# Performance work log

Measured on AMD Instinct MI355X. Metric: run time of the kernel, lower is better.

## Reference

```python
import jax, jax.numpy as jnp
import numpy as np

NUM_HEADS = 8


def setup_inputs() -> dict:
    key = jax.random.key(0)
    ks = jax.random.split(key, 14)
    B, S, E = 4, 2048, 512
    D_EMO = 64
    s = 1.0 / np.sqrt(E)
    inp = {
        "query": jax.random.normal(ks[0], (B, S, E), jnp.float32),
        "key": jax.random.normal(ks[1], (B, S, E), jnp.float32),
        "value": jax.random.normal(ks[2], (B, S, E), jnp.float32),
        "emotional_context": jax.random.normal(ks[3], (B, D_EMO), jnp.float32),
        "Wq": jax.random.normal(ks[4], (E, E), jnp.float32) * s,
        "bq": jnp.zeros((E,), jnp.float32),
        "Wk": jax.random.normal(ks[5], (E, E), jnp.float32) * s,
        "bk": jnp.zeros((E,), jnp.float32),
        "Wv": jax.random.normal(ks[6], (E, E), jnp.float32) * s,
        "bv": jnp.zeros((E,), jnp.float32),
        "Wo": jax.random.normal(ks[7], (E, E), jnp.float32) * s,
        "bo": jnp.zeros((E,), jnp.float32),
        "emo_bias": jax.random.normal(ks[8], (NUM_HEADS, 1, 1), jnp.float32),
    }
    return inp


def reference(query, key, value, emotional_context, Wq, bq, Wk, bk, Wv, bv, Wo, bo, emo_bias):
    B, S, E = query.shape
    H = NUM_HEADS
    D = E // H
    scale = 1.0 / np.sqrt(D).astype(np.float32)

    def proj(x, W, b):  # [B,S,E] -> [B,H,S,D]
        return (x @ W.T + b).reshape(B, S, H, D).transpose(0, 2, 1, 3)

    Q = proj(query, Wq, bq)
    K = proj(key, Wk, bk)
    V = proj(value, Wv, bv)

    # [B,H,S,S] score tensor (the memory-bound hot spot)
    scores = jnp.einsum("bhqd,bhkd->bhqk", Q, K) * scale
    scores = scores + emo_bias[None]  # additive per-head emotional bias
    # multiplicative emotional modulation: sigmoid of mean context, per batch
    mod = 0.5 + 0.5 * jax.nn.sigmoid(emotional_context.mean(axis=-1))  # [B]
    scores = scores * mod[:, None, None, None]

    attn = jax.nn.softmax(scores, axis=-1)
    # dropout(0.1) is identity in eval mode
    attended = jnp.einsum("bhqk,bhkd->bhqd", attn, V)
    attended = attended.transpose(0, 2, 1, 3).reshape(B, S, E)
    output = attended @ Wo.T + bo
    return output, attn.mean(axis=1)
```

## Files before the change

kernel.cpp:

```cpp
#include <hip/hip_runtime.h>

#define BATCH 4
#define SEQ   2048
#define EMB   512
#define HEADS 8
#define HD    64

typedef _Float16 half2_t __attribute__((ext_vector_type(2)));
typedef _Float16 half4_t __attribute__((ext_vector_type(4)));
typedef _Float16 half8_t __attribute__((ext_vector_type(8)));
typedef float    f32x4   __attribute__((ext_vector_type(4)));

#if __has_builtin(__builtin_amdgcn_exp2f)
#define EXP2F(x) __builtin_amdgcn_exp2f(x)
#else
#define EXP2F(x) exp2f(x)
#endif
#define LOG2E 1.44269504088896f

#define PKRTZ(a, b) __builtin_bit_cast(half2_t, __builtin_amdgcn_cvt_pkrtz((a), (b)))

__global__ void mod_kernel(const float* __restrict__ emo, float* __restrict__ modv){
    int lane = threadIdx.x;
    for (int b = 0; b < BATCH; ++b){
        float v = emo[b*64 + lane];
        #pragma unroll
        for (int off = 32; off >= 1; off >>= 1) v += __shfl_xor(v, off, 64);
        if (lane == 0){
            float mean = v * (1.0f/64.0f);
            float sig  = 1.0f/(1.0f + __expf(-mean));
            modv[b] = 0.5f + 0.5f*sig;
        }
    }
}

__device__ inline half8_t cvt8(const float* p){
    float4 v0 = *(const float4*)p;
    float4 v1 = *(const float4*)(p + 4);
    half8_t r;
    r[0]=(_Float16)v0.x; r[1]=(_Float16)v0.y; r[2]=(_Float16)v0.z; r[3]=(_Float16)v0.w;
    r[4]=(_Float16)v1.x; r[5]=(_Float16)v1.y; r[6]=(_Float16)v1.z; r[7]=(_Float16)v1.w;
    return r;
}

__global__ __launch_bounds__(256) void qkv_kernel(
    const float* __restrict__ X0, const float* __restrict__ X1, const float* __restrict__ X2,
    const float* __restrict__ W0, const float* __restrict__ W1, const float* __restrict__ W2,
    const float* __restrict__ b0, const float* __restrict__ b1, const float* __restrict__ b2,
    _Float16* __restrict__ o0, _Float16* __restrict__ o1, _Float16* __restrict__ o2)
{
    const int z = blockIdx.z;
    const float* X    = (z==0) ? X0 : (z==1) ? X1 : X2;
    const float* W    = (z==0) ? W0 : (z==1) ? W1 : W2;
    const float* bias = (z==0) ? b0 : (z==1) ? b1 : b2;
    _Float16*  out    = (z==0) ? o0 : (z==1) ? o1 : o2;

    __shared__ _Float16 lA[128*64];
    __shared__ _Float16 lB[64*64];

    const int tid  = threadIdx.x;
    const int wid  = tid >> 6;
    const int lane = tid & 63;
    const int l16  = lane & 15;
    const int g    = lane >> 4;
    const int l7   = l16 & 7;
    const int mb = blockIdx.x;
    const int nb = blockIdx.y;
    const int wm = (wid >> 1)*64;
    const int wn = (wid & 1)*32;
    const int tR = tid >> 3;
    const int c8 = tid & 7;

    f32x4 acc[4][2] = {};
    for (int ks = 0; ks < 8; ++ks){
        __syncthreads();
        #pragma unroll
        for (int p = 0; p < 4; ++p){
            const int R = p*32 + tR;
            half8_t h = cvt8(X + (size_t)(mb*128 + R)*EMB + ks*64 + c8*8);
            *(half8_t*)(lA + R*64 + ((c8 ^ (R & 7))*8)) = h;
        }
        #pragma unroll
        for (int p = 0; p < 2; ++p){
            const int R = p*32 + tR;
            half8_t h = cvt8(W + (size_t)(nb*64 + R)*EMB + ks*64 + c8*8);
            *(half8_t*)(lB + R*64 + ((c8 ^ (R & 7))*8)) = h;
        }
        __syncthreads();
        #pragma unroll
        for (int u = 0; u < 2; ++u){
            half8_t af[4], bf[2];
            #pragma unroll
            for (int i = 0; i < 4; ++i){
                const int rA = wm + i*16 + l16;
                af[i] = *(half8_t*)(lA + rA*64 + (((u*4 + g) ^ l7)*8));
            }
            #pragma unroll
            for (int j = 0; j < 2; ++j){
                const int rB = wn + j*16 + l16;
                bf[j] = *(half8_t*)(lB + rB*64 + (((u*4 + g) ^ l7)*8));
            }
            #pragma unroll
            for (int i = 0; i < 4; ++i)
                #pragma unroll
                for (int j = 0; j < 2; ++j)
                    acc[i][j] = __builtin_amdgcn_mfma_f32_16x16x32_f16(af[i], bf[j], acc[i][j], 0, 0, 0);
        }
    }
    #pragma unroll
    for (int j = 0; j < 2; ++j){
        const int nn  = nb*64 + wn + j*16 + l16;
        const float bn = bias[nn];
        const int h = nn >> 6, d = nn & 63;
        #pragma unroll
        for (int i = 0; i < 4; ++i){
            #pragma unroll
            for (int r = 0; r < 4; ++r){
                const int m  = mb*128 + wm + i*16 + 4*g + r;
                const int bb2 = m >> 11, s = m & 2047;
                const int bh  = bb2*8 + h;
                const float v = acc[i][j][r] + bn;
                size_t idx;
                if (z == 2)
                    idx = ((size_t)(bh*128 + (s>>4))*2 + (d>>5))*512
                        + (size_t)((((s>>2)&3)*16 + (d&15))*8 + ((d>>4)&1)*4 + (s&3));
                else
                    idx = ((size_t)(bh*128 + (s>>4))*2 + (d>>5))*512
                        + (size_t)((((d>>3)&3)*16 + (s&15))*8 + (d&7));
                out[idx] = (_Float16)v;
            }
        }
    }
}

__global__ __launch_bounds__(256) void pv_kernel(
    const _Float16* __restrict__ Qf, const _Float16* __restrict__ Kf,
    const _Float16* __restrict__ Vf, const float* __restrict__ emo_bias,
    const float* __restrict__ modv, _Float16* __restrict__ attended,
    float* __restrict__ Ldenom)
{
    __shared__ _Float16 lK[2][4096];
    __shared__ _Float16 lV[2][4096];

    const int tid  = threadIdx.x;
    const int lane = tid & 63;
    const int l16  = lane & 15;
    const int g    = lane >> 4;
    const int w    = tid >> 6;
    const int n    = blockIdx.x;
    const int work = (n & 7)*128 + (n >> 3);
    const int qt   = work & 31;
    const int bh   = work >> 5;
    const int b    = bh >> 3, h = bh & 7;
    const int q0   = qt*64 + w*16;

    const float mod = modv[b];
    const float sm2 = 0.125f * mod * LOG2E;
    const float bm2 = emo_bias[h] * mod * LOG2E;

    const size_t fB = (size_t)bh * 128;

    half8_t qf[2];
    #pragma unroll
    for (int c = 0; c < 2; ++c)
        qf[c] = *(const half8_t*)(Qf + ((fB + (q0>>4))*2 + c)*512 + lane*8);

    {
        const _Float16* gk = Kf + (fB)*1024 + tid*16;
        const _Float16* gv = Vf + (fB)*1024 + tid*16;
        *(half8_t*)(&lK[0][tid*16])     = *(const half8_t*)(gk);
        *(half8_t*)(&lK[0][tid*16 + 8]) = *(const half8_t*)(gk + 8);
        *(half8_t*)(&lV[0][tid*16])     = *(const half8_t*)(gv);
        *(half8_t*)(&lV[0][tid*16 + 8]) = *(const half8_t*)(gv + 8);
    }
    __syncthreads();

    f32x4 acc[4] = {};
    float lsum = 0.f;
    int cur = 0;
    for (int grp = 0; grp < SEQ/64; ++grp){
        half8_t rk0, rk1, rv0, rv1;
        if (grp < SEQ/64 - 1){
            const _Float16* gk = Kf + (fB + (size_t)(grp+1)*4)*1024 + tid*16;
            const _Float16* gv = Vf + (fB + (size_t)(grp+1)*4)*1024 + tid*16;
            rk0 = *(const half8_t*)(gk);
            rk1 = *(const half8_t*)(gk + 8);
            rv0 = *(const half8_t*)(gv);
            rv1 = *(const half8_t*)(gv + 8);
        }
        const _Float16* kb = &lK[cur][0];
        const _Float16* vb = &lV[cur][0];
        #pragma unroll
        for (int t = 0; t < 4; ++t){
            half8_t k0 = *(const half8_t*)(kb + (t*2+0)*512 + lane*8);
            half8_t k1 = *(const half8_t*)(kb + (t*2+1)*512 + lane*8);
            f32x4 s = {};
            s = __builtin_amdgcn_mfma_f32_16x16x32_f16(k0, qf[0], s, 0, 0, 0);
            s = __builtin_amdgcn_mfma_f32_16x16x32_f16(k1, qf[1], s, 0, 0, 0);
            float e0 = EXP2F(s[0]*sm2 + bm2);
            float e1 = EXP2F(s[1]*sm2 + bm2);
            float e2 = EXP2F(s[2]*sm2 + bm2);
            float e3 = EXP2F(s[3]*sm2 + bm2);
            lsum += (e0 + e1) + (e2 + e3);
            half2_t plo = PKRTZ(e0, e1), phi = PKRTZ(e2, e3);
            half4_t pf  = __builtin_shufflevector(plo, phi, 0, 1, 2, 3);
            half8_t vp0 = *(const half8_t*)(vb + (t*2+0)*512 + lane*8);
            half8_t vp1 = *(const half8_t*)(vb + (t*2+1)*512 + lane*8);
            half4_t v0 = __builtin_shufflevector(vp0, vp0, 0, 1, 2, 3);
            half4_t v1 = __builtin_shufflevector(vp0, vp0, 4, 5, 6, 7);
            half4_t v2 = __builtin_shufflevector(vp1, vp1, 0, 1, 2, 3);
            half4_t v3 = __builtin_shufflevector(vp1, vp1, 4, 5, 6, 7);
            acc[0] = __builtin_amdgcn_mfma_f32_16x16x16f16(pf, v0, acc[0], 0, 0, 0);
            acc[1] = __builtin_amdgcn_mfma_f32_16x16x16f16(pf, v1, acc[1], 0, 0, 0);
            acc[2] = __builtin_amdgcn_mfma_f32_16x16x16f16(pf, v2, acc[2], 0, 0, 0);
            acc[3] = __builtin_amdgcn_mfma_f32_16x16x16f16(pf, v3, acc[3], 0, 0, 0);
        }
        if (grp < SEQ/64 - 1){
            _Float16* dk = &lK[cur^1][tid*16];
            _Float16* dv = &lV[cur^1][tid*16];
            *(half8_t*)(dk)     = rk0;
            *(half8_t*)(dk + 8) = rk1;
            *(half8_t*)(dv)     = rv0;
            *(half8_t*)(dv + 8) = rv1;
        }
        __syncthreads();
        cur ^= 1;
    }

    lsum += __shfl_xor(lsum, 16, 64);
    lsum += __shfl_xor(lsum, 32, 64);
    if (g == 0) Ldenom[(size_t)bh*SEQ + q0 + l16] = lsum;
    const float inv = 1.0f / lsum;
    float invr[4];
    #pragma unroll
    for (int r = 0; r < 4; ++r)
        invr[r] = __shfl(inv, 4*g + r, 64);
    #pragma unroll
    for (int c = 0; c < 4; ++c)
        #pragma unroll
        for (int r = 0; r < 4; ++r)
            attended[(size_t)(b*SEQ + q0 + 4*g + r)*EMB + h*64 + 16*c + l16]
                = (_Float16)(acc[c][r] * invr[r]);
}

__global__ __launch_bounds__(256) void mean_kernel(
    const _Float16* __restrict__ Qf, const _Float16* __restrict__ Kf,
    const float* __restrict__ emo_bias, const float* __restrict__ modv,
    const float* __restrict__ Ldenom, float* __restrict__ mean_out)
{
    const int tid  = threadIdx.x;
    const int w    = tid >> 6;
    const int lane = tid & 63;
    const int l16  = lane & 15;
    const int g    = lane >> 4;
    const int n    = blockIdx.x;
    const int work = (n & 7)*512 + (n >> 3);
    const int b    = work >> 10;
    const int ky   = (work >> 7) & 7;
    const int qt   = work & 127;
    const int q0   = qt * 16;
    const int k0w  = ky*256 + w*64;

    const float mod = modv[b];
    const float sm2 = 0.125f * mod * LOG2E;

    f32x4 msum[4] = {};
    for (int hp = 0; hp < HEADS/2; ++hp){
        const int h0 = 2*hp, h1 = 2*hp + 1;
        const size_t lo0 = (size_t)(b*HEADS + h0) * SEQ;
        const size_t lo1 = (size_t)(b*HEADS + h1) * SEQ;
        const size_t f0  = (size_t)(b*HEADS + h0) * 128;
        const size_t f1  = (size_t)(b*HEADS + h1) * 128;
        const float bm20 = emo_bias[h0] * mod * LOG2E;
        const float bm21 = emo_bias[h1] * mod * LOG2E;
        half8_t qa0 = *(const half8_t*)(Qf + ((f0 + (q0>>4))*2 + 0)*512 + lane*8);
        half8_t qa1 = *(const half8_t*)(Qf + ((f0 + (q0>>4))*2 + 1)*512 + lane*8);
        half8_t qb0 = *(const half8_t*)(Qf + ((f1 + (q0>>4))*2 + 0)*512 + lane*8);
        half8_t qb1 = *(const half8_t*)(Qf + ((f1 + (q0>>4))*2 + 1)*512 + lane*8);
        float iA[4], iB[4];
        #pragma unroll
        for (int r = 0; r < 4; ++r){
            iA[r] = 1.0f / Ldenom[lo0 + q0 + 4*g + r];
            iB[r] = 1.0f / Ldenom[lo1 + q0 + 4*g + r];
        }
        #pragma unroll
        for (int j = 0; j < 4; ++j){
            const int kc = (k0w >> 4) + j;
            half8_t ka0 = *(const half8_t*)(Kf + ((f0 + kc)*2 + 0)*512 + lane*8);
            half8_t ka1 = *(const half8_t*)(Kf + ((f0 + kc)*2 + 1)*512 + lane*8);
            half8_t kb0 = *(const half8_t*)(Kf + ((f1 + kc)*2 + 0)*512 + lane*8);
            half8_t kb1 = *(const half8_t*)(Kf + ((f1 + kc)*2 + 1)*512 + lane*8);
            f32x4 sA = {}, sB = {};
            sA = __builtin_amdgcn_mfma_f32_16x16x32_f16(qa0, ka0, sA, 0, 0, 0);
            sA = __builtin_amdgcn_mfma_f32_16x16x32_f16(qa1, ka1, sA, 0, 0, 0);
            sB = __builtin_amdgcn_mfma_f32_16x16x32_f16(qb0, kb0, sB, 0, 0, 0);
            sB = __builtin_amdgcn_mfma_f32_16x16x32_f16(qb1, kb1, sB, 0, 0, 0);
            #pragma unroll
            for (int r = 0; r < 4; ++r){
                float pa = EXP2F(sA[r]*sm2 + bm20) * iA[r];
                float pb = EXP2F(sB[r]*sm2 + bm21) * iB[r];
                msum[j][r] += pa + pb;
            }
        }
    }
    #pragma unroll
    for (int j = 0; j < 4; ++j)
        #pragma unroll
        for (int r = 0; r < 4; ++r)
            mean_out[(size_t)(b*SEQ + q0 + 4*g + r)*SEQ + k0w + j*16 + l16]
                = msum[j][r] * (1.0f/HEADS);
}

__global__ __launch_bounds__(256) void outproj_kernel(
    const _Float16* __restrict__ A, const float* __restrict__ W,
    const float* __restrict__ bias, float* __restrict__ out)
{
    __shared__ _Float16 lA[128*64];
    __shared__ _Float16 lB[64*64];

    const int tid  = threadIdx.x;
    const int wid  = tid >> 6;
    const int lane = tid & 63;
    const int l16  = lane & 15;
    const int g    = lane >> 4;
    const int l7   = l16 & 7;
    const int mb = blockIdx.x;
    const int nb = blockIdx.y;
    const int wm = (wid >> 1)*64;
    const int wn = (wid & 1)*32;
    const int tR = tid >> 3;
    const int c8 = tid & 7;

    f32x4 acc[4][2] = {};
    for (int ks = 0; ks < 8; ++ks){
        __syncthreads();
        #pragma unroll
        for (int p = 0; p < 4; ++p){
            const int R = p*32 + tR;
            half8_t h = *(const half8_t*)(A + (size_t)(mb*128 + R)*EMB + ks*64 + c8*8);
            *(half8_t*)(lA + R*64 + ((c8 ^ (R & 7))*8)) = h;
        }
        #pragma unroll
        for (int p = 0; p < 2; ++p){
            const int R = p*32 + tR;
            half8_t h = cvt8(W + (size_t)(nb*64 + R)*EMB + ks*64 + c8*8);
            *(half8_t*)(lB + R*64 + ((c8 ^ (R & 7))*8)) = h;
        }
        __syncthreads();
        #pragma unroll
        for (int u = 0; u < 2; ++u){
            half8_t af[4], bf[2];
            #pragma unroll
            for (int i = 0; i < 4; ++i){
                const int rA = wm + i*16 + l16;
                af[i] = *(half8_t*)(lA + rA*64 + (((u*4 + g) ^ l7)*8));
            }
            #pragma unroll
            for (int j = 0; j < 2; ++j){
                const int rB = wn + j*16 + l16;
                bf[j] = *(half8_t*)(lB + rB*64 + (((u*4 + g) ^ l7)*8));
            }
            #pragma unroll
            for (int i = 0; i < 4; ++i)
                #pragma unroll
                for (int j = 0; j < 2; ++j)
                    acc[i][j] = __builtin_amdgcn_mfma_f32_16x16x32_f16(af[i], bf[j], acc[i][j], 0, 0, 0);
        }
    }
    #pragma unroll
    for (int j = 0; j < 2; ++j){
        const int nn = nb*64 + wn + j*16 + l16;
        const float bn = bias[nn];
        #pragma unroll
        for (int i = 0; i < 4; ++i)
            #pragma unroll
            for (int r = 0; r < 4; ++r){
                const int m = mb*128 + wm + i*16 + 4*g + r;
                out[(size_t)m*EMB + nn] = acc[i][j][r] + bn;
            }
    }
}

extern "C" void kernel_launch(void* const* d_in, const int* in_sizes, int n_in,
                              void* d_out, int out_size, void* d_ws, size_t ws_size,
                              hipStream_t stream)
{
    const float* query = (const float*)d_in[0];
    const float* key_  = (const float*)d_in[1];
    const float* value = (const float*)d_in[2];
    const float* emo   = (const float*)d_in[3];
    const float* Wq = (const float*)d_in[4];
    const float* bq = (const float*)d_in[5];
    const float* Wk = (const float*)d_in[6];
    const float* bk = (const float*)d_in[7];
    const float* Wv = (const float*)d_in[8];
    const float* bv = (const float*)d_in[9];
    const float* Wo = (const float*)d_in[10];
    const float* bo = (const float*)d_in[11];
    const float* emo_bias = (const float*)d_in[12];

    const size_t NTOK = (size_t)BATCH * SEQ * EMB;
    _Float16* ws       = (_Float16*)d_ws;
    _Float16* Qp       = ws;
    _Float16* Kp       = ws + NTOK;
    _Float16* Vt       = ws + 2*NTOK;
    _Float16* attended = ws + 3*NTOK;

    float* out0     = (float*)d_out;
    float* mean_out = out0 + NTOK;
    float* Ldenom   = out0;
    float* modv     = out0 + (size_t)BATCH*HEADS*SEQ;

    mod_kernel<<<1, 64, 0, stream>>>(emo, modv);
    qkv_kernel<<<dim3(64, 8, 3), 256, 0, stream>>>(query, key_, value, Wq, Wk, Wv,
                                                   bq, bk, bv, Qp, Kp, Vt);
    pv_kernel<<<BATCH*HEADS*(SEQ/64), 256, 0, stream>>>(Qp, Kp, Vt, emo_bias, modv, attended, Ldenom);
    mean_kernel<<<BATCH*(SEQ/16)*(SEQ/256), 256, 0, stream>>>(Qp, Kp, emo_bias, modv, Ldenom, mean_out);
    outproj_kernel<<<dim3(64, 8), 256, 0, stream>>>(attended, Wo, bo, out0);
}
```

Baseline: 177.2 us.

## Double-buffer LDS tiles in projection GEMMs and coalesce K/V tile loads

The QKV and output-projection GEMMs now use two LDS buffers and prefetch the next K-slice from global memory into registers while MFMAs run on the current slice. This removes one barrier per iteration and hides global load latency behind compute. In the attention kernel, the K/V tile copy is reorganised so consecutive threads read consecutive 16-byte chunks (tid*8 and tid*8+2048) instead of 32-byte strided pairs, which should improve coalescing. The GEMMs double their LDS use and raise register pressure, which may lower occupancy.

Measured after the change: 177.3 us. No clear change (+0.1%).

```diff
diff --git a/kernel.cpp b/kernel.cpp
--- a/kernel.cpp
+++ b/kernel.cpp
@@ -37,6 +37,13 @@
 __device__ inline half8_t cvt8(const float* p){
     float4 v0 = *(const float4*)p;
     float4 v1 = *(const float4*)(p + 4);
+    half8_t r;
+    r[0]=(_Float16)v0.x; r[1]=(_Float16)v0.y; r[2]=(_Float16)v0.z; r[3]=(_Float16)v0.w;
+    r[4]=(_Float16)v1.x; r[5]=(_Float16)v1.y; r[6]=(_Float16)v1.z; r[7]=(_Float16)v1.w;
+    return r;
+}
+
+__device__ inline half8_t cvt8v(float4 v0, float4 v1){
     half8_t r;
     r[0]=(_Float16)v0.x; r[1]=(_Float16)v0.y; r[2]=(_Float16)v0.z; r[3]=(_Float16)v0.w;
     r[4]=(_Float16)v1.x; r[5]=(_Float16)v1.y; r[6]=(_Float16)v1.z; r[7]=(_Float16)v1.w;
@@ -55,8 +62,8 @@
     const float* bias = (z==0) ? b0 : (z==1) ? b1 : b2;
     _Float16*  out    = (z==0) ? o0 : (z==1) ? o1 : o2;
 
-    __shared__ _Float16 lA[128*64];
-    __shared__ _Float16 lB[64*64];
+    __shared__ _Float16 lA[2][128*64];
+    __shared__ _Float16 lB[2][64*64];
 
     const int tid  = threadIdx.x;
     const int wid  = tid >> 6;
@@ -71,34 +78,50 @@
     const int tR = tid >> 3;
     const int c8 = tid & 7;
 
+    #pragma unroll
+    for (int p = 0; p < 4; ++p){
+        const int R = p*32 + tR;
+        half8_t h = cvt8(X + (size_t)(mb*128 + R)*EMB + c8*8);
+        *(half8_t*)(&lA[0][R*64 + ((c8 ^ (R & 7))*8)]) = h;
+    }
+    #pragma unroll
+    for (int p = 0; p < 2; ++p){
+        const int R = p*32 + tR;
+        half8_t h = cvt8(W + (size_t)(nb*64 + R)*EMB + c8*8);
+        *(half8_t*)(&lB[0][R*64 + ((c8 ^ (R & 7))*8)]) = h;
+    }
+    __syncthreads();
+
     f32x4 acc[4][2] = {};
+    int cur = 0;
     for (int ks = 0; ks < 8; ++ks){
-        __syncthreads();
-        #pragma unroll
-        for (int p = 0; p < 4; ++p){
-            const int R = p*32 + tR;
-            half8_t h = cvt8(X + (size_t)(mb*128 + R)*EMB + ks*64 + c8*8);
-            *(half8_t*)(lA + R*64 + ((c8 ^ (R & 7))*8)) = h;
-        }
-        #pragma unroll
-        for (int p = 0; p < 2; ++p){
-            const int R = p*32 + tR;
-            half8_t h = cvt8(W + (size_t)(nb*64 + R)*EMB + ks*64 + c8*8);
-            *(half8_t*)(lB + R*64 + ((c8 ^ (R & 7))*8)) = h;
-        }
-        __syncthreads();
+        float4 xa0[4], xa1[4], wb0[2], wb1[2];
+        if (ks < 7){
+            #pragma unroll
+            for (int p = 0; p < 4; ++p){
+                const float* px = X + (size_t)(mb*128 + p*32 + tR)*EMB + (ks+1)*64 + c8*8;
+                xa0[p] = *(const float4*)px;
+                xa1[p] = *(const float4*)(px + 4);
+            }
+            #pragma unroll
+            for (int p = 0; p < 2; ++p){
+                const float* pw = W + (size_t)(nb*64 + p*32 + tR)*EMB + (ks+1)*64 + c8*8;
+                wb0[p] = *(const float4*)pw;
+                wb1[p] = *(const float4*)(pw + 4);
+            }
+        }
         #pragma unroll
         for (int u = 0; u < 2; ++u){
             half8_t af[4], bf[2];
             #pragma unroll
             for (int i = 0; i < 4; ++i){
                 const int rA = wm + i*16 + l16;
-                af[i] = *(half8_t*)(lA + rA*64 + (((u*4 + g) ^ l7)*8));
+                af[i] = *(half8_t*)(&lA[cur][rA*64 + (((u*4 + g) ^ l7)*8)]);
             }
             #pragma unroll
             for (int j = 0; j < 2; ++j){
                 const int rB = wn + j*16 + l16;
-                bf[j] = *(half8_t*)(lB + rB*64 + (((u*4 + g) ^ l7)*8));
+                bf[j] = *(half8_t*)(&lB[cur][rB*64 + (((u*4 + g) ^ l7)*8)]);
             }
             #pragma unroll
             for (int i = 0; i < 4; ++i)
@@ -106,6 +129,20 @@
                 for (int j = 0; j < 2; ++j)
                     acc[i][j] = __builtin_amdgcn_mfma_f32_16x16x32_f16(af[i], bf[j], acc[i][j], 0, 0, 0);
         }
+        if (ks < 7){
+            #pragma unroll
+            for (int p = 0; p < 4; ++p){
+                const int R = p*32 + tR;
+                *(half8_t*)(&lA[cur^1][R*64 + ((c8 ^ (R & 7))*8)]) = cvt8v(xa0[p], xa1[p]);
+            }
+            #pragma unroll
+            for (int p = 0; p < 2; ++p){
+                const int R = p*32 + tR;
+                *(half8_t*)(&lB[cur^1][R*64 + ((c8 ^ (R & 7))*8)]) = cvt8v(wb0[p], wb1[p]);
+            }
+        }
+        __syncthreads();
+        cur ^= 1;
     }
     #pragma unroll
     for (int j = 0; j < 2; ++j){
@@ -166,12 +203,12 @@
         qf[c] = *(const half8_t*)(Qf + ((fB + (q0>>4))*2 + c)*512 + lane*8);
 
     {
-        const _Float16* gk = Kf + (fB)*1024 + tid*16;
-        const _Float16* gv = Vf + (fB)*1024 + tid*16;
-        *(half8_t*)(&lK[0][tid*16])     = *(const half8_t*)(gk);
-        *(half8_t*)(&lK[0][tid*16 + 8]) = *(const half8_t*)(gk + 8);
-        *(half8_t*)(&lV[0][tid*16])     = *(const half8_t*)(gv);
-        *(half8_t*)(&lV[0][tid*16 + 8]) = *(const half8_t*)(gv + 8);
+        const _Float16* gk = Kf + fB*1024;
+        const _Float16* gv = Vf + fB*1024;
+        *(half8_t*)(&lK[0][tid*8])        = *(const half8_t*)(gk + tid*8);
+        *(half8_t*)(&lK[0][2048 + tid*8]) = *(const half8_t*)(gk + 2048 + tid*8);
+        *(half8_t*)(&lV[0][tid*8])        = *(const half8_t*)(gv + tid*8);
+        *(half8_t*)(&lV[0][2048 + tid*8]) = *(const half8_t*)(gv + 2048 + tid*8);
     }
     __syncthreads();
 
@@ -181,12 +218,12 @@
     for (int grp = 0; grp < SEQ/64; ++grp){
         half8_t rk0, rk1, rv0, rv1;
         if (grp < SEQ/64 - 1){
-            const _Float16* gk = Kf + (fB + (size_t)(grp+1)*4)*1024 + tid*16;
-            const _Float16* gv = Vf + (fB + (size_t)(grp+1)*4)*1024 + tid*16;
-            rk0 = *(const half8_t*)(gk);
-            rk1 = *(const half8_t*)(gk + 8);
-            rv0 = *(const half8_t*)(gv);
-            rv1 = *(const half8_t*)(gv + 8);
+            const _Float16* gk = Kf + (fB + (size_t)(grp+1)*4)*1024;
+            const _Float16* gv = Vf + (fB + (size_t)(grp+1)*4)*1024;
+            rk0 = *(const half8_t*)(gk + tid*8);
+            rk1 = *(const half8_t*)(gk + 2048 + tid*8);
+            rv0 = *(const half8_t*)(gv + tid*8);
+            rv1 = *(const half8_t*)(gv + 2048 + tid*8);
         }
         const _Float16* kb = &lK[cur][0];
         const _Float16* vb = &lV[cur][0];
@@ -216,12 +253,10 @@
             acc[3] = __builtin_amdgcn_mfma_f32_16x16x16f16(pf, v3, acc[3], 0, 0, 0);
         }
         if (grp < SEQ/64 - 1){
-            _Float16* dk = &lK[cur^1][tid*16];
-            _Float16* dv = &lV[cur^1][tid*16];
-            *(half8_t*)(dk)     = rk0;
-            *(half8_t*)(dk + 8) = rk1;
-            *(half8_t*)(dv)     = rv0;
-            *(half8_t*)(dv + 8) = rv1;
+            *(half8_t*)(&lK[cur^1][tid*8])        = rk0;
+            *(half8_t*)(&lK[cur^1][2048 + tid*8]) = rk1;
+            *(half8_t*)(&lV[cur^1][tid*8])        = rv0;
+            *(half8_t*)(&lV[cur^1][2048 + tid*8]) = rv1;
         }
         __syncthreads();
         cur ^= 1;
@@ -315,8 +350,8 @@
     const _Float16* __restrict__ A, const float* __restrict__ W,
     const float* __restrict__ bias, float* __restrict__ out)
 {
-    __shared__ _Float16 lA[128*64];
-    __shared__ _Float16 lB[64*64];
+    __shared__ _Float16 lA[2][128*64];
+    __shared__ _Float16 lB[2][64*64];
 
     const int tid  = threadIdx.x;
     const int wid  = tid >> 6;
@@ -331,34 +366,48 @@
     const int tR = tid >> 3;
     const int c8 = tid & 7;
 
+    #pragma unroll
+    for (int p = 0; p < 4; ++p){
+        const int R = p*32 + tR;
+        half8_t h = *(const half8_t*)(A + (size_t)(mb*128 + R)*EMB + c8*8);
+        *(half8_t*)(&lA[0][R*64 + ((c8 ^ (R & 7))*8)]) = h;
+    }
+    #pragma unroll
+    for (int p = 0; p < 2; ++p){
+        const int R = p*32 + tR;
+        half8_t h = cvt8(W + (size_t)(nb*64 + R)*EMB + c8*8);
+        *(half8_t*)(&lB[0][R*64 + ((c8 ^ (R & 7))*8)]) = h;
+    }
+    __syncthreads();
+
     f32x4 acc[4][2] = {};
+    int cur = 0;
     for (int ks = 0; ks < 8; ++ks){
-        __syncthreads();
-        #pragma unroll
-        for (int p = 0; p < 4; ++p){
-            const int R = p*32 + tR;
-            half8_t h = *(const half8_t*)(A + (size_t)(mb*128 + R)*EMB + ks*64 + c8*8);
-            *(half8_t*)(lA + R*64 + ((c8 ^ (R & 7))*8)) = h;
-        }
-        #pragma unroll
-        for (int p = 0; p < 2; ++p){
-            const int R = p*32 + tR;
-            half8_t h = cvt8(W + (size_t)(nb*64 + R)*EMB + ks*64 + c8*8);
-            *(half8_t*)(lB + R*64 + ((c8 ^ (R & 7))*8)) = h;
-        }
-        __syncthreads();
+        half8_t ra[4];
+        float4 wb0[2], wb1[2];
+        if (ks < 7){
+            #pragma unroll
+            for (int p = 0; p < 4; ++p)
+                ra[p] = *(const half8_t*)(A + (size_t)(mb*128 + p*32 + tR)*EMB + (ks+1)*64 + c8*8);
+            #pragma unroll
+            for (int p = 0; p < 2; ++p){
+                const float* pw = W + (size_t)(nb*64 + p*32 + tR)*EMB + (ks+1)*64 + c8*8;
+                wb0[p] = *(const float4*)pw;
+                wb1[p] = *(const float4*)(pw + 4);
+            }
+        }
         #pragma unroll
         for (int u = 0; u < 2; ++u){
             half8_t af[4], bf[2];
             #pragma unroll
             for (int i = 0; i < 4; ++i){
                 const int rA = wm + i*16 + l16;
-                af[i] = *(half8_t*)(lA + rA*64 + (((u*4 + g) ^ l7)*8));
+                af[i] = *(half8_t*)(&lA[cur][rA*64 + (((u*4 + g) ^ l7)*8)]);
             }
             #pragma unroll
             for (int j = 0; j < 2; ++j){
                 const int rB = wn + j*16 + l16;
-                bf[j] = *(half8_t*)(lB + rB*64 + (((u*4 + g) ^ l7)*8));
+                bf[j] = *(half8_t*)(&lB[cur][rB*64 + (((u*4 + g) ^ l7)*8)]);
             }
             #pragma unroll
             for (int i = 0; i < 4; ++i)
@@ -366,6 +415,20 @@
                 for (int j = 0; j < 2; ++j)
                     acc[i][j] = __builtin_amdgcn_mfma_f32_16x16x32_f16(af[i], bf[j], acc[i][j], 0, 0, 0);
         }
+        if (ks < 7){
+            #pragma unroll
+            for (int p = 0; p < 4; ++p){
+                const int R = p*32 + tR;
+                *(half8_t*)(&lA[cur^1][R*64 + ((c8 ^ (R & 7))*8)]) = ra[p];
+            }
+            #pragma unroll
+            for (int p = 0; p < 2; ++p){
+                const int R = p*32 + tR;
+                *(half8_t*)(&lB[cur^1][R*64 + ((c8 ^ (R & 7))*8)]) = cvt8v(wb0[p], wb1[p]);
+            }
+        }
+        __syncthreads();
+        cur ^= 1;
     }
     #pragma unroll
     for (int j = 0; j < 2; ++j){
```
